# Performance work log

Measured on AMD Instinct MI355X. Metric: run time of the kernel, lower is better.

The kernel has to match this reference:

```python
import jax, jax.numpy as jnp
import numpy as np


def _rgcn_layer(h, Wr, Ws, src, dst, rel, norm):
    # h: [N,d], Wr: [R,d,d] per-relation weight, Ws: [d,d] self-loop weight
    N, d = h.shape
    R = Wr.shape[0]
    E = src.shape[0]
    msg = jnp.zeros((E, d), h.dtype)
    for r in range(R):  # R is small/static; transform-then-gather per relation
        hW = h @ Wr[r]              # [N,d]
        msg = jnp.where((rel == r)[:, None], hW[src], msg)  # [E,d]
    agg = jax.ops.segment_sum(msg * norm[:, None], dst, num_segments=N)
    return jax.nn.relu(agg + h @ Ws)


def _calc_score(emb, w_relation, es, er, eo):
    # DistMult-style bilinear score: s^T W_r o per target edge
    s = emb[es]                     # [T,d]
    o = emb[eo]                     # [T,d]
    R = w_relation.shape[0]
    sW = jnp.zeros_like(s)
    for r in range(R):
        sW = jnp.where((er == r)[:, None], s @ w_relation[r], sW)
    return jnp.sum(sW * o, axis=-1)  # [T]


def setup_inputs() -> dict:
    key = jax.random.key(0)
    ks = jax.random.split(key, 16)
    N, E, T, d, R, L = 20000, 160000, 50000, 768, 8, 2
    sc = 1.0 / np.sqrt(d)
    return {
        "node_feat": jax.random.normal(ks[0], (N, d), jnp.float32),
        "edge_norm": jax.random.uniform(ks[1], (E,), jnp.float32),
        "W_rel": jax.random.normal(ks[2], (L, R, d, d), jnp.float32) * sc,
        "W_self": jax.random.normal(ks[3], (L, d, d), jnp.float32) * sc,
        "w_relation": jax.random.normal(ks[4], (R, d, d), jnp.float32) * sc,
        "src": jax.random.randint(ks[5], (E,), 0, N, jnp.int32),
        "dst": jax.random.randint(ks[6], (E,), 0, N, jnp.int32),
        "rel": jax.random.randint(ks[7], (E,), 0, R, jnp.int32),
        "pos_src": jax.random.randint(ks[8], (T,), 0, N, jnp.int32),
        "pos_rel": jax.random.randint(ks[9], (T,), 0, R, jnp.int32),
        "pos_dst": jax.random.randint(ks[10], (T,), 0, N, jnp.int32),
        "neg_src": jax.random.randint(ks[11], (T,), 0, N, jnp.int32),
        "neg_rel": jax.random.randint(ks[12], (T,), 0, R, jnp.int32),
        "neg_dst": jax.random.randint(ks[13], (T,), 0, N, jnp.int32),
    }


def reference(node_feat, edge_norm, W_rel, W_self, w_relation,
              src, dst, rel, pos_src, pos_rel, pos_dst,
              neg_src, neg_rel, neg_dst):
    h = node_feat
    L = W_rel.shape[0]
    for l in range(L):
        h = _rgcn_layer(h, W_rel[l], W_self[l], src, dst, rel, edge_norm)
    es = jnp.concatenate([pos_src, neg_src])
    er = jnp.concatenate([pos_rel, neg_rel])
    eo = jnp.concatenate([pos_dst, neg_dst])
    score = _calc_score(h, w_relation, es, er, eo)  # [2T]
    return score
```

## Files before the change

kernel.cpp:

```cpp
#include <hip/hip_runtime.h>

typedef float f32x4 __attribute__((ext_vector_type(4)));
typedef __bf16 bf16x8 __attribute__((ext_vector_type(8)));
typedef unsigned short u16x8 __attribute__((ext_vector_type(8)));
typedef unsigned short u16x4 __attribute__((ext_vector_type(4)));

static __device__ __forceinline__ unsigned short f2bf(float f) {
  unsigned int x = __builtin_bit_cast(unsigned int, f);
  x += 0x7FFFu + ((x >> 16) & 1u);
  return (unsigned short)(x >> 16);
}
static __device__ __forceinline__ float bf2f(unsigned short h) {
  unsigned int x = ((unsigned int)h) << 16;
  return __builtin_bit_cast(float, x);
}

static __device__ __forceinline__ void gload_lds16(const unsigned short* g,
                                                   unsigned short* l) {
  __builtin_amdgcn_global_load_lds(
      (const __attribute__((address_space(1))) void*)g,
      (__attribute__((address_space(3))) void*)l, 16, 0, 0);
}

__global__ __launch_bounds__(256) void k_f32_to_bf16(
    const float* __restrict__ in, unsigned short* __restrict__ out, int n4) {
  int i = blockIdx.x * 256 + threadIdx.x;
  if (i >= n4) return;
  float4 v = reinterpret_cast<const float4*>(in)[i];
  u16x4 o = {f2bf(v.x), f2bf(v.y), f2bf(v.z), f2bf(v.w)};
  reinterpret_cast<u16x4*>(out)[i] = o;
}

__global__ __launch_bounds__(256) void k_transpose_w(
    const float* __restrict__ in, unsigned short* __restrict__ out, int RG) {
  __shared__ float tile[32][33];
  const int D = 768;
  int z = blockIdx.z;
  int j = z % RG, grp = z / RG;
  const float* A = in + (size_t)z * D * D;
  const size_t ld = (size_t)RG * D;
  unsigned short* O = out + (size_t)grp * D * ld + (size_t)j * D;
  int nt = blockIdx.x * 32, kt = blockIdx.y * 32;
  int tx = threadIdx.x, ty = threadIdx.y;
#pragma unroll
  for (int i = 0; i < 4; ++i)
    tile[ty + i * 8][tx] = A[(size_t)(kt + ty + i * 8) * D + nt + tx];
  __syncthreads();
#pragma unroll
  for (int i = 0; i < 4; ++i)
    O[(size_t)(nt + ty + i * 8) * ld + kt + tx] = f2bf(tile[tx][ty + i * 8]);
}

__global__ __launch_bounds__(256) void k_hist(const int* __restrict__ dst,
                                              const int* __restrict__ rel,
                                              int* __restrict__ cnt, int E, int NV) {
  int e = blockIdx.x * 256 + threadIdx.x;
  if (e < E) atomicAdd(&cnt[rel[e] * NV + dst[e]], 1);
}

__global__ __launch_bounds__(256) void k_part(const int* __restrict__ cnt,
                                              int* __restrict__ bsum, int n) {
  __shared__ int wsums[4];
  int blk = blockIdx.x, tid = threadIdx.x;
  int base = blk * 1024 + tid * 4;
  int s = 0;
#pragma unroll
  for (int j = 0; j < 4; ++j) {
    int i = base + j;
    if (i < n) s += cnt[i];
  }
#pragma unroll
  for (int d = 1; d < 64; d <<= 1) s += __shfl_xor(s, d, 64);
  if ((tid & 63) == 0) wsums[tid >> 6] = s;
  __syncthreads();
  if (tid == 0) bsum[blk] = wsums[0] + wsums[1] + wsums[2] + wsums[3];
}

__global__ __launch_bounds__(1024) void k_scan_b(const int* __restrict__ bsum,
                                                 int* __restrict__ bscan, int nb,
                                                 int* __restrict__ off_total) {
  __shared__ int wpre[16];
  int tid = threadIdx.x, lane = tid & 63, w = tid >> 6;
  int v = (tid < nb) ? bsum[tid] : 0;
  int inc = v;
#pragma unroll
  for (int d = 1; d < 64; d <<= 1) {
    int t = __shfl_up(inc, d, 64);
    if (lane >= d) inc += t;
  }
  if (lane == 63) wpre[w] = inc;
  __syncthreads();
  if (w == 0) {
    int vv = (lane < 16) ? wpre[lane] : 0;
    int p = vv;
#pragma unroll
    for (int d = 1; d < 16; d <<= 1) {
      int t = __shfl_up(p, d, 64);
      if (lane >= d) p += t;
    }
    if (lane < 16) wpre[lane] = p - vv;
  }
  __syncthreads();
  if (tid < nb) bscan[tid] = wpre[w] + inc - v;
  if (tid == 1023) *off_total = wpre[15] + inc;
}

__global__ __launch_bounds__(256) void k_scan_f(const int* __restrict__ cnt,
                                                const int* __restrict__ bscan,
                                                int* __restrict__ off, int n) {
  __shared__ int wpre[4];
  int blk = blockIdx.x, tid = threadIdx.x, lane = tid & 63, w = tid >> 6;
  int base = blk * 1024 + tid * 4;
  int v[4];
  int s = 0;
#pragma unroll
  for (int j = 0; j < 4; ++j) {
    int i = base + j;
    v[j] = (i < n) ? cnt[i] : 0;
    s += v[j];
  }
  int inc = s;
#pragma unroll
  for (int d = 1; d < 64; d <<= 1) {
    int t = __shfl_up(inc, d, 64);
    if (lane >= d) inc += t;
  }
  if (lane == 63) wpre[w] = inc;
  __syncthreads();
  int wb = 0;
  for (int j = 0; j < w; ++j) wb += wpre[j];
  int run = bscan[blk] + wb + (inc - s);
#pragma unroll
  for (int j = 0; j < 4; ++j) {
    int i = base + j;
    if (i < n) off[i] = run;
    run += v[j];
  }
}

__global__ __launch_bounds__(256) void k_bucket(
    const int* __restrict__ src, const int* __restrict__ dst,
    const int* __restrict__ rel, const float* __restrict__ norm,
    const int* __restrict__ off, int* __restrict__ fill,
    int* __restrict__ spack, float* __restrict__ snorm, int E, int NV) {
  int e = blockIdx.x * 256 + threadIdx.x;
  if (e >= E) return;
  int key = rel[e] * NV + dst[e];
  int slot = off[key] + atomicAdd(&fill[key], 1);
  spack[slot] = src[e];
  snorm[slot] = norm[e];
}

__global__ __launch_bounds__(256) void k_gather(
    const unsigned short* __restrict__ h, const int* __restrict__ off,
    const int* __restrict__ spack, const float* __restrict__ snorm,
    unsigned short* __restrict__ Acat, int NV, int r0, int r1, int ld) {
  int v = (blockIdx.x * 256 + threadIdx.x) >> 6;
  int lane = threadIdx.x & 63;
  int col = lane * 4;
  for (int r = r0; r < r1; ++r) {
    float a[12];
#pragma unroll
    for (int j = 0; j < 12; ++j) a[j] = 0.f;
    if (v < NV) {
      int beg = off[r * NV + v], end = off[r * NV + v + 1];
      for (int p = beg; p < end; ++p) {
        const unsigned short* row = h + (size_t)spack[p] * 768 + col;
        float nm = snorm[p];
#pragma unroll
        for (int c = 0; c < 3; ++c) {
          u16x4 vv = *reinterpret_cast<const u16x4*>(row + c * 256);
#pragma unroll
          for (int j = 0; j < 4; ++j) a[c * 4 + j] += nm * bf2f(vv[j]);
        }
      }
    }
    unsigned short* orow = Acat + (size_t)v * ld + (size_t)(r - r0) * 768 + col;
#pragma unroll
    for (int c = 0; c < 3; ++c) {
      u16x4 o = {f2bf(a[c * 4 + 0]), f2bf(a[c * 4 + 1]),
                 f2bf(a[c * 4 + 2]), f2bf(a[c * 4 + 3])};
      *reinterpret_cast<u16x4*>(orow + c * 256) = o;
    }
  }
}

#define STAGE_A(BUF, HALF, TT)                                                   \
  do {                                                                           \
    const unsigned short* _s =                                                   \
        A + (size_t)(m0 + (HALF) * 128 + srow) * K + (size_t)(TT) * 64 + gcol;   \
    gload_lds16(_s, &As[BUF][HALF][w << 3][0]);                                  \
    gload_lds16(_s + (size_t)64 * K, &As[BUF][HALF][64 + (w << 3)][0]);          \
  } while (0)
#define STAGE_B(BUF, HALF, TT)                                                   \
  do {                                                                           \
    const unsigned short* _s =                                                   \
        B + (size_t)(n0 + (HALF) * 128 + srow) * K + (size_t)(TT) * 64 + gcol;   \
    gload_lds16(_s, &Bs[BUF][HALF][w << 3][0]);                                  \
    gload_lds16(_s + (size_t)64 * K, &Bs[BUF][HALF][64 + (w << 3)][0]);          \
  } while (0)

template <int EPI>
__global__ __launch_bounds__(512, 2) void k_gemm_tn(
    const unsigned short* __restrict__ A, const unsigned short* __restrict__ B,
    void* __restrict__ Cp, const float* __restrict__ C0,
    int M, int N, int K, int MT, int NT) {
  __shared__ unsigned short As[2][2][128][64];
  __shared__ unsigned short Bs[2][2][128][64];
  const int tid = threadIdx.x;
  const int lane = tid & 63;
  const int w = tid >> 6;
  const int wr = w >> 2;
  const int wc = w & 3;
  const int lr = lane & 15, lg = lane >> 4;

  int bid = blockIdx.x;
  const int per = 8 * NT;
  int grp = bid / per, rem = bid % per;
  int mstart = grp * 8;
  int gsz = MT - mstart; if (gsz > 8) gsz = 8;
  const int mt = mstart + rem % gsz;
  const int ntile = rem / gsz;
  const int m0 = mt * 256, n0 = ntile * 256;

  const int srow = tid >> 3;
  const int gcol = (((tid & 7) ^ (tid >> 3)) & 7) * 8;

  f32x4 acc[2][2][4][2] = {};
  const int nk = K >> 6;

  STAGE_A(0, 0, 0);
  STAGE_B(0, 1, 0);
  STAGE_A(0, 1, 0);
  STAGE_B(0, 0, 0);
  if (nk > 1) {
    STAGE_A(1, 0, 1);
    STAGE_B(1, 1, 1);
  }

  bf16x8 af[4][2], bv[2][2][2];
  for (int t = 0; t < nk; ++t) {
    const int buf = t & 1;
    if (t + 1 < nk)
      asm volatile("s_waitcnt vmcnt(4)" ::: "memory");
    else
      asm volatile("s_waitcnt vmcnt(0)" ::: "memory");
    __builtin_amdgcn_s_barrier();
    asm volatile("" ::: "memory");
#pragma unroll
    for (int i = 0; i < 4; ++i)
#pragma unroll
      for (int kk = 0; kk < 2; ++kk)
        af[i][kk] = *reinterpret_cast<const bf16x8*>(
            &As[buf][0][wr * 64 + i * 16 + lr][((lg + 4 * kk) ^ (lr & 7)) * 8]);
#pragma unroll
    for (int nb = 0; nb < 2; ++nb)
#pragma unroll
      for (int j = 0; j < 2; ++j)
#pragma unroll
        for (int kk = 0; kk < 2; ++kk)
          bv[nb][j][kk] = *reinterpret_cast<const bf16x8*>(
              &Bs[buf][nb][wc * 32 + j * 16 + lr][((lg + 4 * kk) ^ (lr & 7)) * 8]);
    if (t + 1 < nk) {
      STAGE_A(buf ^ 1, 1, t + 1);
      STAGE_B(buf ^ 1, 0, t + 1);
    }
    __builtin_amdgcn_s_setprio(1);
#pragma unroll
    for (int i = 0; i < 4; ++i)
#pragma unroll
      for (int nb = 0; nb < 2; ++nb)
#pragma unroll
        for (int j = 0; j < 2; ++j)
#pragma unroll
          for (int kk = 0; kk < 2; ++kk)
            acc[0][nb][i][j] = __builtin_amdgcn_mfma_f32_16x16x32_bf16(
                af[i][kk], bv[nb][j][kk], acc[0][nb][i][j], 0, 0, 0);
    __builtin_amdgcn_s_setprio(0);
    asm volatile("" ::: "memory");
    __builtin_amdgcn_s_barrier();
    asm volatile("" ::: "memory");
#pragma unroll
    for (int i = 0; i < 4; ++i)
#pragma unroll
      for (int kk = 0; kk < 2; ++kk)
        af[i][kk] = *reinterpret_cast<const bf16x8*>(
            &As[buf][1][wr * 64 + i * 16 + lr][((lg + 4 * kk) ^ (lr & 7)) * 8]);
    if (t + 2 < nk) {
      STAGE_A(buf, 0, t + 2);
      STAGE_B(buf, 1, t + 2);
    }
    __builtin_amdgcn_s_setprio(1);
#pragma unroll
    for (int i = 0; i < 4; ++i)
#pragma unroll
      for (int nb = 0; nb < 2; ++nb)
#pragma unroll
        for (int j = 0; j < 2; ++j)
#pragma unroll
          for (int kk = 0; kk < 2; ++kk)
            acc[1][nb][i][j] = __builtin_amdgcn_mfma_f32_16x16x32_bf16(
                af[i][kk], bv[nb][j][kk], acc[1][nb][i][j], 0, 0, 0);
    __builtin_amdgcn_s_setprio(0);
  }

#pragma unroll
  for (int ma = 0; ma < 2; ++ma)
#pragma unroll
    for (int i = 0; i < 4; ++i)
#pragma unroll
      for (int q = 0; q < 4; ++q) {
        int r = m0 + ma * 128 + wr * 64 + i * 16 + lg * 4 + q;
        if (r >= M) continue;
#pragma unroll
        for (int nb = 0; nb < 2; ++nb)
#pragma unroll
          for (int j = 0; j < 2; ++j) {
            int cn = n0 + nb * 128 + wc * 32 + j * 16 + lr;
            float v = acc[ma][nb][i][j][q];
            size_t idx = (size_t)r * N + cn;
            if (EPI == 0) {
              ((unsigned short*)Cp)[idx] = f2bf(v);
            } else if (EPI == 1) {
              v += C0[idx];
              v = v > 0.f ? v : 0.f;
              ((unsigned short*)Cp)[idx] = f2bf(v);
            } else if (EPI == 2) {
              ((float*)Cp)[idx] = v;
            } else {
              ((float*)Cp)[idx] = v + C0[idx];
            }
          }
      }
}

__global__ __launch_bounds__(256) void k_score(
    const unsigned short* __restrict__ SW, const unsigned short* __restrict__ emb,
    const int* __restrict__ ps, const int* __restrict__ pr, const int* __restrict__ pd,
    const int* __restrict__ ns, const int* __restrict__ nr, const int* __restrict__ nd,
    float* __restrict__ out, int T, int r0, int r1, int ldSW) {
  int t = (blockIdx.x * 256 + threadIdx.x) >> 6;
  if (t >= 2 * T) return;
  int s, r, o;
  if (t < T) { s = ps[t]; r = pr[t]; o = pd[t]; }
  else       { s = ns[t - T]; r = nr[t - T]; o = nd[t - T]; }
  if (r < r0 || r >= r1) return;
  int lane = threadIdx.x & 63;
  int col = lane * 4;
  const unsigned short* a = SW + (size_t)s * ldSW + (size_t)(r - r0) * 768 + col;
  const unsigned short* b = emb + (size_t)o * 768 + col;
  float acc = 0.f;
#pragma unroll
  for (int c = 0; c < 3; ++c) {
    u16x4 va = *reinterpret_cast<const u16x4*>(a + c * 256);
    u16x4 vb = *reinterpret_cast<const u16x4*>(b + c * 256);
#pragma unroll
    for (int j = 0; j < 4; ++j) acc += bf2f(va[j]) * bf2f(vb[j]);
  }
#pragma unroll
  for (int off = 32; off > 0; off >>= 1) acc += __shfl_down(acc, off, 64);
  if (lane == 0) out[t] = acc;
}

extern "C" void kernel_launch(void* const* d_in, const int* in_sizes, int n_in,
                              void* d_out, int out_size, void* d_ws, size_t ws_size,
                              hipStream_t stream) {
  const float* node_feat = (const float*)d_in[0];
  const float* edge_norm = (const float*)d_in[1];
  const float* W_rel = (const float*)d_in[2];
  const float* W_self = (const float*)d_in[3];
  const float* w_relation = (const float*)d_in[4];
  const int* src = (const int*)d_in[5];
  const int* dst = (const int*)d_in[6];
  const int* rel = (const int*)d_in[7];
  const int* pos_src = (const int*)d_in[8];
  const int* pos_rel = (const int*)d_in[9];
  const int* pos_dst = (const int*)d_in[10];
  const int* neg_src = (const int*)d_in[11];
  const int* neg_rel = (const int*)d_in[12];
  const int* neg_dst = (const int*)d_in[13];

  const int D = 768;
  const int NV = in_sizes[0] / D;
  const int E = in_sizes[1];
  const int L = in_sizes[3] / (D * D);
  const int R = in_sizes[4] / (D * D);
  const int T = in_sizes[8];
  const int Mpad = (NV + 255) & ~255;
  const int RN = R * NV;
  const int NB = (RN + 1023) / 1024;

  auto align_up = [](size_t x) { return (x + 255) & ~(size_t)255; };
  size_t sz_wt_rel = align_up((size_t)L * R * D * D * 2);
  size_t sz_wt_self = align_up((size_t)L * D * D * 2);
  size_t sz_wt_score = align_up((size_t)R * D * D * 2);
  size_t sz_h = align_up((size_t)Mpad * D * 2);
  size_t sz_agg = align_up((size_t)Mpad * D * 4);
  size_t sz_cntfill = align_up((size_t)2 * RN * 4);
  size_t sz_off = align_up((size_t)(RN + 8) * 4);
  size_t sz_sp = align_up((size_t)E * 4);
  size_t sz_bs = align_up((size_t)2 * (NB + 8) * 4);
  size_t fixed = sz_wt_rel + sz_wt_self + sz_wt_score + sz_h + sz_agg +
                 sz_cntfill + sz_off + 2 * sz_sp + sz_bs;
  int RG = 4;
  while (RG > 1 && fixed + align_up((size_t)Mpad * RG * D * 2) > ws_size) RG >>= 1;
  const int NGRP = R / RG;

  char* wp = (char*)d_ws;
  unsigned short* wt_rel = (unsigned short*)wp; wp += sz_wt_rel;
  unsigned short* wt_self = (unsigned short*)wp; wp += sz_wt_self;
  unsigned short* wt_score = (unsigned short*)wp; wp += sz_wt_score;
  unsigned short* h = (unsigned short*)wp; wp += sz_h;
  float* agg = (float*)wp; wp += sz_agg;
  int* cnt = (int*)wp; int* fill = cnt + RN; wp += sz_cntfill;
  int* off = (int*)wp; wp += sz_off;
  int* spack = (int*)wp; wp += sz_sp;
  float* snorm = (float*)wp; wp += sz_sp;
  int* bsum = (int*)wp; int* bscan = bsum + NB + 4; wp += sz_bs;
  unsigned short* Acat = (unsigned short*)wp;

  dim3 tb32(32, 8);
  k_f32_to_bf16<<<(NV * D / 4 + 255) / 256, 256, 0, stream>>>(node_feat, h, NV * D / 4);
  if (Mpad > NV)
    hipMemsetAsync(h + (size_t)NV * D, 0, (size_t)(Mpad - NV) * D * 2, stream);
  k_transpose_w<<<dim3(24, 24, L * R), tb32, 0, stream>>>(W_rel, wt_rel, RG);
  k_transpose_w<<<dim3(24, 24, L), tb32, 0, stream>>>(W_self, wt_self, 1);
  k_transpose_w<<<dim3(24, 24, R), tb32, 0, stream>>>(w_relation, wt_score, 1);

  hipMemsetAsync(cnt, 0, (size_t)2 * RN * 4, stream);
  k_hist<<<(E + 255) / 256, 256, 0, stream>>>(dst, rel, cnt, E, NV);
  k_part<<<NB, 256, 0, stream>>>(cnt, bsum, RN);
  k_scan_b<<<1, 1024, 0, stream>>>(bsum, bscan, NB, off + RN);
  k_scan_f<<<NB, 256, 0, stream>>>(cnt, bscan, off, RN);
  k_bucket<<<(E + 255) / 256, 256, 0, stream>>>(src, dst, rel, edge_norm, off, fill,
                                                spack, snorm, E, NV);

  const int MT = Mpad / 256;
  const int KG = RG * D;
  const int gblocks = Mpad / 4;
  for (int l = 0; l < L; ++l) {
    k_gemm_tn<2><<<MT * 3, 512, 0, stream>>>(
        h, wt_self + (size_t)l * D * D, agg, nullptr, NV, D, D, MT, 3);
    for (int gi = 0; gi < NGRP; ++gi) {
      k_gather<<<gblocks, 256, 0, stream>>>(h, off, spack, snorm, Acat, NV,
                                            gi * RG, gi * RG + RG, KG);
      const unsigned short* Bw = wt_rel + (size_t)(l * NGRP + gi) * D * KG;
      if (gi == NGRP - 1)
        k_gemm_tn<1><<<MT * 3, 512, 0, stream>>>(Acat, Bw, h, agg, NV, D, KG, MT, 3);
      else
        k_gemm_tn<3><<<MT * 3, 512, 0, stream>>>(Acat, Bw, agg, agg, NV, D, KG, MT, 3);
    }
  }
  for (int gi = 0; gi < NGRP; ++gi) {
    k_gemm_tn<0><<<MT * RG * 3, 512, 0, stream>>>(
        h, wt_score + (size_t)gi * RG * D * D, Acat, nullptr, NV, KG, D, MT, RG * 3);
    k_score<<<(2 * T + 3) / 4, 256, 0, stream>>>(Acat, h, pos_src, pos_rel, pos_dst,
                                                 neg_src, neg_rel, neg_dst,
                                                 (float*)d_out, T, gi * RG,
                                                 gi * RG + RG, KG);
  }
}
```

Before: 883.2 us.

## Add 8-phase pipelined GEMM kernel with finer-grained staging for layer GEMMs

Adds k_gemm8, a GEMM variant that splits each K-step into four quadrant MFMA phases. Each phase issues a smaller global-to-LDS stage and waits on its own barrier, so loads are spread more evenly across compute. LDS fragment reads are reused across phases (bv0/bv1 held, af reloaded once) and lgkmcnt waits plus scheduling barriers are made explicit. The layer GEMMs now use this kernel, while the score GEMM keeps the old one. The trade-off is twice as many barriers per K-step and more live B registers.

Result: slower. 936.6 us (+6.0%).

```diff
diff --git a/kernel.cpp b/kernel.cpp
--- a/kernel.cpp
+++ b/kernel.cpp
@@ -199,6 +199,61 @@
     gload_lds16(_s, &Bs[BUF][HALF][w << 3][0]);                                  \
     gload_lds16(_s + (size_t)64 * K, &Bs[BUF][HALF][64 + (w << 3)][0]);          \
   } while (0)
+#define GEMM_PRE()                                                               \
+  const int tid = threadIdx.x;                                                   \
+  const int lane = tid & 63;                                                     \
+  const int w = tid >> 6;                                                        \
+  const int wr = w >> 2;                                                         \
+  const int wc = w & 3;                                                          \
+  const int lr = lane & 15, lg = lane >> 4;                                      \
+  int bid = blockIdx.x;                                                          \
+  const int per = 8 * NT;                                                        \
+  int grp = bid / per, rem = bid % per;                                          \
+  int mstart = grp * 8;                                                          \
+  int gsz = MT - mstart;                                                         \
+  if (gsz > 8) gsz = 8;                                                          \
+  const int mt = mstart + rem % gsz;                                             \
+  const int ntile = rem / gsz;                                                   \
+  const int m0 = mt * 256, n0 = ntile * 256;                                     \
+  const int srow = tid >> 3;                                                     \
+  const int gcol = (((tid & 7) ^ (tid >> 3)) & 7) * 8;                           \
+  const int nk = K >> 6;
+#define GEMM_EPILOGUE()                                                          \
+  _Pragma("unroll") for (int ma = 0; ma < 2; ++ma)                               \
+  _Pragma("unroll") for (int i = 0; i < 4; ++i)                                  \
+  _Pragma("unroll") for (int q = 0; q < 4; ++q) {                                \
+    int r = m0 + ma * 128 + wr * 64 + i * 16 + lg * 4 + q;                       \
+    if (r >= M) continue;                                                        \
+    _Pragma("unroll") for (int nb = 0; nb < 2; ++nb)                             \
+    _Pragma("unroll") for (int j = 0; j < 2; ++j) {                              \
+      int cn = n0 + nb * 128 + wc * 32 + j * 16 + lr;                            \
+      float v = acc[ma][nb][i][j][q];                                            \
+      size_t idx = (size_t)r * N + cn;                                           \
+      if (EPI == 0) {                                                            \
+        ((unsigned short*)Cp)[idx] = f2bf(v);                                    \
+      } else if (EPI == 1) {                                                     \
+        v += C0[idx];                                                            \
+        v = v > 0.f ? v : 0.f;                                                   \
+        ((unsigned short*)Cp)[idx] = f2bf(v);                                    \
+      } else if (EPI == 2) {                                                     \
+        ((float*)Cp)[idx] = v;                                                   \
+      } else {                                                                   \
+        ((float*)Cp)[idx] = v + C0[idx];                                         \
+      }                                                                          \
+    }                                                                            \
+  }
+
+#define R_BV6(BUF)                                                               \
+  _Pragma("unroll") for (int nb = 0; nb < 2; ++nb)                               \
+  _Pragma("unroll") for (int j = 0; j < 2; ++j)                                  \
+  _Pragma("unroll") for (int kk = 0; kk < 2; ++kk)                               \
+      bv[nb][j][kk] = *reinterpret_cast<const bf16x8*>(                          \
+          &Bs[BUF][nb][wc * 32 + j * 16 + lr][((lg + 4 * kk) ^ (lr & 7)) * 8]);
+#define R_AF6(BUF, HALF)                                                         \
+  _Pragma("unroll") for (int i = 0; i < 4; ++i)                                  \
+  _Pragma("unroll") for (int kk = 0; kk < 2; ++kk)                               \
+      af[i][kk] = *reinterpret_cast<const bf16x8*>(                              \
+          &As[BUF][HALF][wr * 64 + i * 16 + lr][((lg + 4 * kk) ^ (lr & 7)) * 8]);
 
 template <int EPI>
 __global__ __launch_bounds__(512, 2) void k_gemm_tn(
@@ -207,27 +262,8 @@
     int M, int N, int K, int MT, int NT) {
   __shared__ unsigned short As[2][2][128][64];
   __shared__ unsigned short Bs[2][2][128][64];
-  const int tid = threadIdx.x;
-  const int lane = tid & 63;
-  const int w = tid >> 6;
-  const int wr = w >> 2;
-  const int wc = w & 3;
-  const int lr = lane & 15, lg = lane >> 4;
-
-  int bid = blockIdx.x;
-  const int per = 8 * NT;
-  int grp = bid / per, rem = bid % per;
-  int mstart = grp * 8;
-  int gsz = MT - mstart; if (gsz > 8) gsz = 8;
-  const int mt = mstart + rem % gsz;
-  const int ntile = rem / gsz;
-  const int m0 = mt * 256, n0 = ntile * 256;
-
-  const int srow = tid >> 3;
-  const int gcol = (((tid & 7) ^ (tid >> 3)) & 7) * 8;
-
+  GEMM_PRE();
   f32x4 acc[2][2][4][2] = {};
-  const int nk = K >> 6;
 
   STAGE_A(0, 0, 0);
   STAGE_B(0, 1, 0);
@@ -247,20 +283,8 @@
       asm volatile("s_waitcnt vmcnt(0)" ::: "memory");
     __builtin_amdgcn_s_barrier();
     asm volatile("" ::: "memory");
-#pragma unroll
-    for (int i = 0; i < 4; ++i)
-#pragma unroll
-      for (int kk = 0; kk < 2; ++kk)
-        af[i][kk] = *reinterpret_cast<const bf16x8*>(
-            &As[buf][0][wr * 64 + i * 16 + lr][((lg + 4 * kk) ^ (lr & 7)) * 8]);
-#pragma unroll
-    for (int nb = 0; nb < 2; ++nb)
-#pragma unroll
-      for (int j = 0; j < 2; ++j)
-#pragma unroll
-        for (int kk = 0; kk < 2; ++kk)
-          bv[nb][j][kk] = *reinterpret_cast<const bf16x8*>(
-              &Bs[buf][nb][wc * 32 + j * 16 + lr][((lg + 4 * kk) ^ (lr & 7)) * 8]);
+    R_AF6(buf, 0);
+    R_BV6(buf);
     if (t + 1 < nk) {
       STAGE_A(buf ^ 1, 1, t + 1);
       STAGE_B(buf ^ 1, 0, t + 1);
@@ -280,12 +304,7 @@
     asm volatile("" ::: "memory");
     __builtin_amdgcn_s_barrier();
     asm volatile("" ::: "memory");
-#pragma unroll
-    for (int i = 0; i < 4; ++i)
-#pragma unroll
-      for (int kk = 0; kk < 2; ++kk)
-        af[i][kk] = *reinterpret_cast<const bf16x8*>(
-            &As[buf][1][wr * 64 + i * 16 + lr][((lg + 4 * kk) ^ (lr & 7)) * 8]);
+    R_AF6(buf, 1);
     if (t + 2 < nk) {
       STAGE_A(buf, 0, t + 2);
       STAGE_B(buf, 1, t + 2);
@@ -303,35 +322,87 @@
                 af[i][kk], bv[nb][j][kk], acc[1][nb][i][j], 0, 0, 0);
     __builtin_amdgcn_s_setprio(0);
   }
-
-#pragma unroll
-  for (int ma = 0; ma < 2; ++ma)
-#pragma unroll
-    for (int i = 0; i < 4; ++i)
-#pragma unroll
-      for (int q = 0; q < 4; ++q) {
-        int r = m0 + ma * 128 + wr * 64 + i * 16 + lg * 4 + q;
-        if (r >= M) continue;
-#pragma unroll
-        for (int nb = 0; nb < 2; ++nb)
-#pragma unroll
-          for (int j = 0; j < 2; ++j) {
-            int cn = n0 + nb * 128 + wc * 32 + j * 16 + lr;
-            float v = acc[ma][nb][i][j][q];
-            size_t idx = (size_t)r * N + cn;
-            if (EPI == 0) {
-              ((unsigned short*)Cp)[idx] = f2bf(v);
-            } else if (EPI == 1) {
-              v += C0[idx];
-              v = v > 0.f ? v : 0.f;
-              ((unsigned short*)Cp)[idx] = f2bf(v);
-            } else if (EPI == 2) {
-              ((float*)Cp)[idx] = v;
-            } else {
-              ((float*)Cp)[idx] = v + C0[idx];
-            }
-          }
-      }
+  GEMM_EPILOGUE();
+}
+
+#define R_BV8(DST, BUF, HALF)                                                    \
+  _Pragma("unroll") for (int j = 0; j < 2; ++j)                                  \
+  _Pragma("unroll") for (int kk = 0; kk < 2; ++kk)                               \
+      DST[j][kk] = *reinterpret_cast<const bf16x8*>(                             \
+          &Bs[BUF][HALF][wc * 32 + j * 16 + lr][((lg + 4 * kk) ^ (lr & 7)) * 8]);
+#define MB16(MA, NB, BV)                                                         \
+  __builtin_amdgcn_s_setprio(1);                                                 \
+  _Pragma("unroll") for (int i = 0; i < 4; ++i)                                  \
+  _Pragma("unroll") for (int j = 0; j < 2; ++j)                                  \
+  _Pragma("unroll") for (int kk = 0; kk < 2; ++kk)                               \
+      acc[MA][NB][i][j] = __builtin_amdgcn_mfma_f32_16x16x32_bf16(               \
+          af[i][kk], BV[j][kk], acc[MA][NB][i][j], 0, 0, 0);                     \
+  __builtin_amdgcn_s_setprio(0);
+#define MIDSYNC                                                                  \
+  asm volatile("" ::: "memory");                                                 \
+  __builtin_amdgcn_s_barrier();                                                  \
+  asm volatile("s_waitcnt lgkmcnt(0)" ::: "memory");                             \
+  __builtin_amdgcn_sched_barrier(0);
+#define ENDBAR                                                                   \
+  asm volatile("" ::: "memory");                                                 \
+  __builtin_amdgcn_s_barrier();                                                  \
+  asm volatile("" ::: "memory");
+
+template <int EPI>
+__global__ __launch_bounds__(512, 2) void k_gemm8(
+    const unsigned short* __restrict__ A, const unsigned short* __restrict__ B,
+    void* __restrict__ Cp, const float* __restrict__ C0,
+    int M, int N, int K, int MT, int NT) {
+  __shared__ unsigned short As[2][2][128][64];
+  __shared__ unsigned short Bs[2][2][128][64];
+  GEMM_PRE();
+  f32x4 acc[2][2][4][2] = {};
+  bf16x8 af[4][2], bv0[2][2], bv1[2][2];
+
+  STAGE_A(0, 0, 0);
+  STAGE_B(0, 0, 0);
+  STAGE_B(0, 1, 0);
+  STAGE_A(0, 1, 0);
+  if (nk > 1) {
+    STAGE_A(1, 0, 1);
+    STAGE_B(1, 0, 1);
+    STAGE_B(1, 1, 1);
+    asm volatile("s_waitcnt vmcnt(6)" ::: "memory");
+  } else {
+    asm volatile("s_waitcnt vmcnt(0)" ::: "memory");
+  }
+  __builtin_amdgcn_s_barrier();
+  asm volatile("" ::: "memory");
+
+  for (int t = 0; t < nk; ++t) {
+    const int b = t & 1;
+    R_AF6(b, 0);
+    R_BV8(bv0, b, 0);
+    if (t + 1 < nk) STAGE_A(b ^ 1, 1, t + 1);
+    MIDSYNC;
+    MB16(0, 0, bv0);
+    ENDBAR;
+    R_BV8(bv1, b, 1);
+    if (t + 2 < nk) STAGE_A(b, 0, t + 2);
+    MIDSYNC;
+    MB16(0, 1, bv1);
+    ENDBAR;
+    R_AF6(b, 1);
+    if (t + 2 < nk) STAGE_B(b, 0, t + 2);
+    MIDSYNC;
+    MB16(1, 1, bv1);
+    ENDBAR;
+    if (t + 2 < nk) {
+      STAGE_B(b, 1, t + 2);
+      asm volatile("s_waitcnt vmcnt(6)" ::: "memory");
+    } else {
+      asm volatile("s_waitcnt vmcnt(0)" ::: "memory");
+    }
+    MIDSYNC;
+    MB16(1, 0, bv0);
+    ENDBAR;
+  }
+  GEMM_EPILOGUE();
 }
 
 __global__ __launch_bounds__(256) void k_score(
@@ -439,16 +510,16 @@
   const int KG = RG * D;
   const int gblocks = Mpad / 4;
   for (int l = 0; l < L; ++l) {
-    k_gemm_tn<2><<<MT * 3, 512, 0, stream>>>(
+    k_gemm8<2><<<MT * 3, 512, 0, stream>>>(
         h, wt_self + (size_t)l * D * D, agg, nullptr, NV, D, D, MT, 3);
     for (int gi = 0; gi < NGRP; ++gi) {
       k_gather<<<gblocks, 256, 0, stream>>>(h, off, spack, snorm, Acat, NV,
                                             gi * RG, gi * RG + RG, KG);
       const unsigned short* Bw = wt_rel + (size_t)(l * NGRP + gi) * D * KG;
       if (gi == NGRP - 1)
-        k_gemm_tn<1><<<MT * 3, 512, 0, stream>>>(Acat, Bw, h, agg, NV, D, KG, MT, 3);
+        k_gemm8<1><<<MT * 3, 512, 0, stream>>>(Acat, Bw, h, agg, NV, D, KG, MT, 3);
       else
-        k_gemm_tn<3><<<MT * 3, 512, 0, stream>>>(Acat, Bw, agg, agg, NV, D, KG, MT, 3);
+        k_gemm8<3><<<MT * 3, 512, 0, stream>>>(Acat, Bw, agg, agg, NV, D, KG, MT, 3);
     }
   }
   for (int gi = 0; gi < NGRP; ++gi) {
```
